# Kernel optimization log

Hardware: AMD Instinct MI355X
Metric: run time of the kernel (lower is better)

The kernel has to match this reference:

```python
import jax, jax.numpy as jnp
from jax import lax
import numpy as np

EXPLORED_MAP = 1  # MC.EXPLORED_MAP channel index


def _disk(radius: int) -> np.ndarray:
    # skimage.morphology.disk(radius): Euclidean disk structuring element
    y, x = np.ogrid[-radius:radius + 1, -radius:radius + 1]
    return (x * x + y * y <= radius * radius).astype(np.float32)


def setup_inputs() -> dict:
    key = jax.random.key(0)
    B, C, M = 8, 24, 960  # (batch, 8 + num_sem_categories, map, map)
    # explored-map channel is binary {0,1}; other channels arbitrary
    map_features = jax.random.randint(key, (B, C, M, M), 0, 2).astype(jnp.float32)
    dilate_explored_kernel = jnp.asarray(_disk(10))[None, None]  # (1,1,21,21)
    select_border_kernel = jnp.asarray(_disk(1))[None, None]     # (1,1,3,3)
    return {
        "map_features": map_features,
        "dilate_explored_kernel": dilate_explored_kernel,
        "select_border_kernel": select_border_kernel,
    }


def _conv_same(x, k):
    # x: (B,1,M,M), k: (1,1,kh,kw); SAME padding, stride 1
    return lax.conv_general_dilated(
        x, k, window_strides=(1, 1), padding="SAME",
        dimension_numbers=("NCHW", "OIHW", "NCHW"))


def binary_erosion(x, k):
    return jnp.clip(_conv_same(x, k) - jnp.sum(k) + 1.0, 0.0, 1.0)


def binary_dilation(x, k):
    return jnp.clip(_conv_same(x, k), 0.0, 1.0)


def reference(map_features, dilate_explored_kernel, select_border_kernel):
    # frontier = unexplored cells
    frontier = (map_features[:, EXPLORED_MAP:EXPLORED_MAP + 1] == 0).astype(map_features.dtype)
    eroded = binary_erosion(frontier, dilate_explored_kernel)
    goal_map = binary_dilation(eroded, select_border_kernel) - eroded  # border of eroded frontier
    return goal_map  # (B, 1, M, M)
```

## Files before the change

kernel.cpp:

```cpp
#include <hip/hip_runtime.h>
#include <stdint.h>


#define MDIM 960
#define NW 15
#define TILE 8
#define RSTAGE (TILE + 22)
#define EROWS (TILE + 2)
#define NTHREADS 256
#define NBATCH 8
#define NCHAN 24
#define EXPLORED_CH 1

__global__ __launch_bounds__(NTHREADS) void frontier_kernel(
    const float* __restrict__ in, float* __restrict__ out)
{
    __shared__ uint64_t sF[RSTAGE][NW];
    __shared__ uint64_t sH[6][RSTAGE][NW];
    __shared__ uint64_t sE[EROWS][NW];

    const int bx   = blockIdx.x;
    const int b    = bx / (MDIM / TILE);
    const int tile = bx % (MDIM / TILE);
    const int i0   = tile * TILE;
    const int tid  = threadIdx.x;
    const int lane = tid & 63;
    const int wv   = tid >> 6;

    const size_t chan = (size_t)MDIM * MDIM;
    const float* src = in + ((size_t)b * NCHAN + EXPLORED_CH) * chan;

    for (int t = wv; t < RSTAGE * NW; t += NTHREADS / 64) {
        int l = t / NW, wd = t % NW;
        int g = i0 - 11 + l;
        uint64_t m = 0;
        if (g >= 0 && g < MDIM) {
            float v = src[(size_t)g * MDIM + wd * 64 + lane];
            m = __ballot(v == 0.0f);
        }
        if (lane == 0) sF[l][wd] = m;
    }
    __syncthreads();

    for (int t = tid; t < RSTAGE * NW; t += NTHREADS) {
        int l = t / NW, wd = t % NW;
        uint64_t a  = (wd > 0)      ? sF[l][wd - 1] : 0ull;
        uint64_t bb = sF[l][wd];
        uint64_t c  = (wd < NW - 1) ? sF[l][wd + 1] : 0ull;
        #pragma unroll
        for (int k = 1; k <= 10; ++k) {
            uint64_t da = (a >> 1) | (bb << 63);
            uint64_t db = (bb >> 1) | (c << 63);
            uint64_t dc = (c >> 1);
            uint64_t ua = (a << 1);
            uint64_t ub = (bb << 1) | (a >> 63);
            uint64_t uc = (c << 1) | (bb >> 63);
            a  &= da & ua;
            bb &= db & ub;
            c  &= dc & uc;
            if (k == 4)  sH[0][l][wd] = bb;
            if (k == 6)  sH[1][l][wd] = bb;
            if (k == 7)  sH[2][l][wd] = bb;
            if (k == 8)  sH[3][l][wd] = bb;
            if (k == 9)  sH[4][l][wd] = bb;
            if (k == 10) sH[5][l][wd] = bb;
        }
    }
    __syncthreads();

    for (int t = tid; t < EROWS * NW; t += NTHREADS) {
        int r = t / NW, wd = t % NW;
        uint64_t e = sF[r][wd] & sF[r + 20][wd];
        e &= sH[0][r + 1][wd] & sH[0][r + 19][wd];
        e &= sH[1][r + 2][wd] & sH[1][r + 18][wd];
        e &= sH[2][r + 3][wd] & sH[2][r + 17][wd];
        e &= sH[3][r + 4][wd] & sH[3][r + 16][wd];
        e &= sH[3][r + 5][wd] & sH[3][r + 15][wd];
        e &= sH[4][r + 6][wd] & sH[4][r + 14][wd];
        e &= sH[4][r + 7][wd] & sH[4][r + 13][wd];
        e &= sH[4][r + 8][wd] & sH[4][r + 12][wd];
        e &= sH[4][r + 9][wd] & sH[4][r + 11][wd];
        e &= sH[5][r + 10][wd];
        sE[r][wd] = e;
    }
    __syncthreads();

    float* dst = out + (size_t)b * chan;
    for (int t = tid; t < TILE * (MDIM / 4); t += NTHREADS) {
        int ro = t / (MDIM / 4), c4 = t % (MDIM / 4);
        int c0 = c4 * 4;
        float vj[4];
        #pragma unroll
        for (int j = 0; j < 4; ++j) {
            int col = c0 + j;
            int wd = col >> 6, sh = col & 63;
            unsigned e  = (unsigned)((sE[ro + 1][wd] >> sh) & 1);
            unsigned n  = (unsigned)((sE[ro    ][wd] >> sh) & 1);
            unsigned s  = (unsigned)((sE[ro + 2][wd] >> sh) & 1);
            unsigned lf = (col > 0)
                ? (unsigned)((sE[ro + 1][(col - 1) >> 6] >> ((col - 1) & 63)) & 1) : 0u;
            unsigned rt = (col < MDIM - 1)
                ? (unsigned)((sE[ro + 1][(col + 1) >> 6] >> ((col + 1) & 63)) & 1) : 0u;
            unsigned d = e | n | s | lf | rt;
            vj[j] = (float)(d & (e ^ 1u));
        }
        float4 v = make_float4(vj[0], vj[1], vj[2], vj[3]);
        *(float4*)(dst + (size_t)(i0 + ro) * MDIM + c0) = v;
    }
}

extern "C" void kernel_launch(void* const* d_in, const int* in_sizes, int n_in,
                              void* d_out, int out_size, void* d_ws, size_t ws_size,
                              hipStream_t stream)
{
    const float* mapf = (const float*)d_in[0];
    float* out = (float*)d_out;
    dim3 grid(NBATCH * (MDIM / TILE));
    frontier_kernel<<<grid, NTHREADS, 0, stream>>>(mapf, out);
}
```

Before: 800.2 us.

## Split bit-packing of explored map into separate kernel writing to workspace

Adds a first kernel that packs each row of the explored channel into 64-bit ballot masks once and writes them to the workspace. The morphology kernel then loads the packed bits instead of re-reading the float rows. Previously each 8-row tile re-read its 30-row halo, so every input row was read from global memory several times. The cost is an extra kernel launch and a small round trip through the workspace.

```diff
diff --git a/kernel.cpp b/kernel.cpp
--- a/kernel.cpp
+++ b/kernel.cpp
@@ -11,9 +11,36 @@
 #define NBATCH 8
 #define NCHAN 24
 #define EXPLORED_CH 1
+#define ROWS_TOTAL (NBATCH * MDIM)
+#define PACK_BLOCKS 480
 
-__global__ __launch_bounds__(NTHREADS) void frontier_kernel(
-    const float* __restrict__ in, float* __restrict__ out)
+__global__ __launch_bounds__(NTHREADS) void frontier_pack_kernel(
+    const float* __restrict__ in, uint64_t* __restrict__ ws)
+{
+    const int wave = blockIdx.x * (NTHREADS / 64) + (threadIdx.x >> 6);
+    const int lane = threadIdx.x & 63;
+    #pragma unroll
+    for (int rr = 0; rr < 4; ++rr) {
+        const int R = wave * 4 + rr;
+        const int b = R / MDIM, row = R % MDIM;
+        const float* src = in + ((size_t)b * NCHAN + EXPLORED_CH) * MDIM * MDIM
+                              + (size_t)row * MDIM;
+        uint64_t w[NW];
+        #pragma unroll
+        for (int j = 0; j < NW; ++j) {
+            float v = src[j * 64 + lane];
+            w[j] = __ballot(v == 0.0f);
+        }
+        if (lane == 0) {
+            uint64_t* dst = ws + (size_t)R * NW;
+            #pragma unroll
+            for (int j = 0; j < NW; ++j) dst[j] = w[j];
+        }
+    }
+}
+
+__global__ __launch_bounds__(NTHREADS) void frontier_morph_kernel(
+    const uint64_t* __restrict__ ws, float* __restrict__ out)
 {
     __shared__ uint64_t sF[RSTAGE][NW];
     __shared__ uint64_t sH[6][RSTAGE][NW];
@@ -24,21 +51,12 @@
     const int tile = bx % (MDIM / TILE);
     const int i0   = tile * TILE;
     const int tid  = threadIdx.x;
-    const int lane = tid & 63;
-    const int wv   = tid >> 6;
 
-    const size_t chan = (size_t)MDIM * MDIM;
-    const float* src = in + ((size_t)b * NCHAN + EXPLORED_CH) * chan;
-
-    for (int t = wv; t < RSTAGE * NW; t += NTHREADS / 64) {
+    const uint64_t* pk = ws + (size_t)b * MDIM * NW;
+    for (int t = tid; t < RSTAGE * NW; t += NTHREADS) {
         int l = t / NW, wd = t % NW;
         int g = i0 - 11 + l;
-        uint64_t m = 0;
-        if (g >= 0 && g < MDIM) {
-            float v = src[(size_t)g * MDIM + wd * 64 + lane];
-            m = __ballot(v == 0.0f);
-        }
-        if (lane == 0) sF[l][wd] = m;
+        sF[l][wd] = (g >= 0 && g < MDIM) ? pk[(size_t)g * NW + wd] : 0ull;
     }
     __syncthreads();
 
@@ -85,7 +103,7 @@
     }
     __syncthreads();
 
-    float* dst = out + (size_t)b * chan;
+    float* dst = out + (size_t)b * MDIM * MDIM;
     for (int t = tid; t < TILE * (MDIM / 4); t += NTHREADS) {
         int ro = t / (MDIM / 4), c4 = t % (MDIM / 4);
         int c0 = c4 * 4;
@@ -115,6 +133,8 @@
 {
     const float* mapf = (const float*)d_in[0];
     float* out = (float*)d_out;
-    dim3 grid(NBATCH * (MDIM / TILE));
-    frontier_kernel<<<grid, NTHREADS, 0, stream>>>(mapf, out);
+    uint64_t* ws = (uint64_t*)d_ws;
+
+    frontier_pack_kernel<<<dim3(PACK_BLOCKS), NTHREADS, 0, stream>>>(mapf, ws);
+    frontier_morph_kernel<<<dim3(NBATCH * (MDIM / TILE)), NTHREADS, 0, stream>>>(ws, out);
 }
```

New measurement: 754.0 us. -5.8%, faster.
